# Kernel optimization log

Hardware: AMD Instinct MI355X
Metric: run time of the kernel (lower is better)

## Reference

```python
import jax, jax.numpy as jnp
import numpy as np

D_MODEL, N_HEADS, D_FF = 1024, 16, 4096
D_K = D_MODEL // N_HEADS
EPS = 1e-6


def _layernorm(x, alpha, bias):
    # Source uses mean and UNBIASED std (torch default), and adds eps to std (not var).
    mean = jnp.mean(x, axis=-1, keepdims=True)
    std = jnp.std(x, axis=-1, keepdims=True, ddof=1)
    return alpha * (x - mean) / (std + EPS) + bias


def setup_inputs() -> dict:
    key = jax.random.key(0)
    ks = jax.random.split(key, 16)
    B, S = 2, 2048
    s = 1.0 / np.sqrt(D_MODEL)
    inp = {
        "x": jax.random.normal(ks[0], (B, S, D_MODEL), dtype=jnp.float32),
        "mask": jnp.ones((1, 1, S, S), dtype=jnp.int32),
        # Linear weights stored as [d_in, d_out]
        "Wq": jax.random.normal(ks[1], (D_MODEL, D_MODEL), dtype=jnp.float32) * s,
        "bq": jnp.zeros((D_MODEL,), dtype=jnp.float32),
        "Wk": jax.random.normal(ks[2], (D_MODEL, D_MODEL), dtype=jnp.float32) * s,
        "bk": jnp.zeros((D_MODEL,), dtype=jnp.float32),
        "Wv": jax.random.normal(ks[3], (D_MODEL, D_MODEL), dtype=jnp.float32) * s,
        "bv": jnp.zeros((D_MODEL,), dtype=jnp.float32),
        "Wo": jax.random.normal(ks[4], (D_MODEL, D_MODEL), dtype=jnp.float32) * s,
        "bo": jnp.zeros((D_MODEL,), dtype=jnp.float32),
        "W1": jax.random.normal(ks[5], (D_MODEL, D_FF), dtype=jnp.float32) * s,
        "b1": jnp.zeros((D_FF,), dtype=jnp.float32),
        "W2": jax.random.normal(ks[6], (D_FF, D_MODEL), dtype=jnp.float32) / np.sqrt(D_FF),
        "b2": jnp.zeros((D_MODEL,), dtype=jnp.float32),
        "alpha1": jnp.ones((1,), dtype=jnp.float32),
        "beta1": jnp.zeros((1,), dtype=jnp.float32),
        "alpha2": jnp.ones((1,), dtype=jnp.float32),
        "beta2": jnp.zeros((1,), dtype=jnp.float32),
    }
    return inp


def reference(x, mask, Wq, bq, Wk, bk, Wv, bv, Wo, bo, W1, b1, W2, b2,
              alpha1, beta1, alpha2, beta2):
    # --- residual 1: pre-norm self-attention (dropout = identity in eval) ---
    xn = _layernorm(x, alpha1, beta1)
    B, S, _ = xn.shape
    q = (xn @ Wq + bq).reshape(B, S, N_HEADS, D_K).transpose(0, 2, 1, 3)  # [B,H,S,Dk]
    k = (xn @ Wk + bk).reshape(B, S, N_HEADS, D_K).transpose(0, 2, 1, 3)
    v = (xn @ Wv + bv).reshape(B, S, N_HEADS, D_K).transpose(0, 2, 1, 3)
    scores = jnp.einsum('bhqd,bhkd->bhqk', q, k) / np.sqrt(D_K)  # [B,H,S,S]
    scores = jnp.where(mask == 0, jnp.float32(-1e9), scores)
    attn = jax.nn.softmax(scores, axis=-1)
    ctx = jnp.einsum('bhqk,bhkd->bhqd', attn, v)
    ctx = ctx.transpose(0, 2, 1, 3).reshape(B, S, D_MODEL)
    attn_out = ctx @ Wo + bo
    x = x + attn_out

    # --- residual 2: pre-norm feed-forward ---
    xn = _layernorm(x, alpha2, beta2)
    ff = jax.nn.relu(xn @ W1 + b1) @ W2 + b2
    return x + ff
```

## Files before the change

kernel.cpp:

```cpp
#include <hip/hip_runtime.h>
#include <hip/hip_bf16.h>
#include <math.h>

#define SEQ   2048
#define BATCH 2
#define DMODEL 1024
#define NH    16
#define DKH   64
#define DFF   4096

typedef __attribute__((ext_vector_type(8))) short s16x8;
typedef __attribute__((ext_vector_type(4))) float f32x4;

__device__ __forceinline__ unsigned short f2bf(float f) {
  __hip_bfloat16 h = __float2bfloat16(f);
  return __builtin_bit_cast(unsigned short, h);
}

__device__ __forceinline__ unsigned cvt_pk_bf16(float lo, float hi) {
  unsigned r;
  asm("v_cvt_pk_bf16_f32 %0, %1, %2" : "=v"(r) : "v"(lo), "v"(hi));
  return r;
}

#define GLOAD16(g, l)                                                        \
  __builtin_amdgcn_global_load_lds(                                          \
      (const __attribute__((address_space(1))) void*)(g),                    \
      (__attribute__((address_space(3))) void*)(l), 16, 0, 0)

__global__ __launch_bounds__(256) void transpose_all_kernel(
    const float* __restrict__ Wq, const float* __restrict__ Wk,
    const float* __restrict__ Wv, const float* __restrict__ Wo,
    const float* __restrict__ W1, const float* __restrict__ W2,
    unsigned short* __restrict__ wq_t, unsigned short* __restrict__ wk_t,
    unsigned short* __restrict__ wv_t, unsigned short* __restrict__ wo_t,
    unsigned short* __restrict__ w1_t, unsigned short* __restrict__ w2_t) {
  const int id = blockIdx.x;
  const float* W; unsigned short* Wt; int K, N, t;
  if (id < 1024) {
    const int w = id >> 8; t = id & 255; K = DMODEL; N = DMODEL;
    W  = (w == 0) ? Wq : (w == 1) ? Wk : (w == 2) ? Wv : Wo;
    Wt = (w == 0) ? wq_t : (w == 1) ? wk_t : (w == 2) ? wv_t : wo_t;
  } else if (id < 2048) {
    t = id - 1024; K = DMODEL; N = DFF; W = W1; Wt = w1_t;
  } else {
    t = id - 2048; K = DFF; N = DMODEL; W = W2; Wt = w2_t;
  }
  const int nx = N / 64;
  const int n0 = (t % nx) * 64, k0 = (t / nx) * 64;
  __shared__ float tile[64][65];
  const int tx = threadIdx.x & 15, ty = threadIdx.x >> 4;
#pragma unroll
  for (int kk = 0; kk < 4; ++kk) {
    const int r = kk * 16 + ty;
    const float4 v = *reinterpret_cast<const float4*>(&W[(size_t)(k0 + r) * N + n0 + tx * 4]);
    tile[r][tx * 4 + 0] = v.x;
    tile[r][tx * 4 + 1] = v.y;
    tile[r][tx * 4 + 2] = v.z;
    tile[r][tx * 4 + 3] = v.w;
  }
  __syncthreads();
#pragma unroll
  for (int nn = 0; nn < 4; ++nn) {
    const int n = nn * 16 + ty;
    ushort4 o;
    o.x = f2bf(tile[tx * 4 + 0][n]);
    o.y = f2bf(tile[tx * 4 + 1][n]);
    o.z = f2bf(tile[tx * 4 + 2][n]);
    o.w = f2bf(tile[tx * 4 + 3][n]);
    *reinterpret_cast<ushort4*>(&Wt[(size_t)(n0 + n) * K + k0 + tx * 4]) = o;
  }
}

__global__ __launch_bounds__(256) void layernorm_kernel(
    const float* __restrict__ x, unsigned short* __restrict__ xn,
    const float* __restrict__ alpha, const float* __restrict__ beta) {
  const int row = blockIdx.x;
  const float4 v = reinterpret_cast<const float4*>(x + (size_t)row * DMODEL)[threadIdx.x];
  float s  = v.x + v.y + v.z + v.w;
  float ss = v.x * v.x + v.y * v.y + v.z * v.z + v.w * v.w;
#pragma unroll
  for (int off = 32; off; off >>= 1) {
    s  += __shfl_down(s, off);
    ss += __shfl_down(ss, off);
  }
  __shared__ float red[8];
  const int wv = threadIdx.x >> 6;
  if ((threadIdx.x & 63) == 0) { red[wv] = s; red[4 + wv] = ss; }
  __syncthreads();
  s  = red[0] + red[1] + red[2] + red[3];
  ss = red[4] + red[5] + red[6] + red[7];
  const float mean = s * (1.0f / DMODEL);
  float var = (ss - (float)DMODEL * mean * mean) * (1.0f / (DMODEL - 1));
  var = fmaxf(var, 0.0f);
  const float inv = alpha[0] / (sqrtf(var) + 1e-6f);
  const float b = beta[0] - mean * inv;
  ushort4 o;
  o.x = f2bf(v.x * inv + b);
  o.y = f2bf(v.y * inv + b);
  o.z = f2bf(v.z * inv + b);
  o.w = f2bf(v.w * inv + b);
  reinterpret_cast<ushort4*>(xn + (size_t)row * DMODEL)[threadIdx.x] = o;
}

template <bool RELU, bool RES, bool BIASM>
__global__ __launch_bounds__(256) void gemm_kernel(
    const unsigned short* __restrict__ A, const unsigned short* __restrict__ Bt,
    const float* __restrict__ bias, const float* __restrict__ res,
    void* __restrict__ out, int M, int N, int K, int ny) {
  __shared__ unsigned short a_lds[128][40];
  __shared__ unsigned short b_lds[128][40];
  const int bid = blockIdx.x;
  const int by = bid % ny, bx = bid / ny;
  const int m0 = by * 128, n0 = bx * 128;
  const int tid = threadIdx.x;
  const int lane = tid & 63, wave = tid >> 6;
  const int wm = wave >> 1, wn = wave & 1;
  const int l15 = lane & 15, lg = lane >> 4;
  const int srow = tid >> 2, scol = (tid & 3) * 8;

  f32x4 acc[4][4] = {};

  for (int k0 = 0; k0 < K; k0 += 32) {
    const int4 a0 = *reinterpret_cast<const int4*>(A + (size_t)(m0 + srow) * K + k0 + scol);
    const int4 a1 = *reinterpret_cast<const int4*>(A + (size_t)(m0 + srow + 64) * K + k0 + scol);
    const int4 b0 = *reinterpret_cast<const int4*>(Bt + (size_t)(n0 + srow) * K + k0 + scol);
    const int4 b1 = *reinterpret_cast<const int4*>(Bt + (size_t)(n0 + srow + 64) * K + k0 + scol);
    __syncthreads();
    *reinterpret_cast<int4*>(&a_lds[srow][scol])      = a0;
    *reinterpret_cast<int4*>(&a_lds[srow + 64][scol]) = a1;
    *reinterpret_cast<int4*>(&b_lds[srow][scol])      = b0;
    *reinterpret_cast<int4*>(&b_lds[srow + 64][scol]) = b1;
    __syncthreads();
    s16x8 af[4], bfr[4];
#pragma unroll
    for (int m = 0; m < 4; ++m)
      af[m] = *reinterpret_cast<const s16x8*>(&a_lds[wm * 64 + m * 16 + l15][lg * 8]);
#pragma unroll
    for (int n = 0; n < 4; ++n)
      bfr[n] = *reinterpret_cast<const s16x8*>(&b_lds[wn * 64 + n * 16 + l15][lg * 8]);
#pragma unroll
    for (int m = 0; m < 4; ++m)
#pragma unroll
      for (int n = 0; n < 4; ++n)
        acc[m][n] = __builtin_amdgcn_mfma_f32_16x16x32_bf16(af[m], bfr[n], acc[m][n], 0, 0, 0);
  }

#pragma unroll
  for (int m = 0; m < 4; ++m) {
#pragma unroll
    for (int n = 0; n < 4; ++n) {
      const int col = n0 + wn * 64 + n * 16 + l15;
      const float bcol = (bias && !BIASM) ? bias[col] : 0.0f;
#pragma unroll
      for (int r = 0; r < 4; ++r) {
        const int row = m0 + wm * 64 + m * 16 + 4 * lg + r;
        float v = acc[m][n][r] + (BIASM ? bias[row] : bcol);
        if (RELU) v = fmaxf(v, 0.0f);
        if (RES) {
          reinterpret_cast<float*>(out)[(size_t)row * N + col] =
              v + res[(size_t)row * N + col];
        } else {
          reinterpret_cast<unsigned short*>(out)[(size_t)row * N + col] = f2bf(v);
        }
      }
    }
  }
}

__global__ __launch_bounds__(512) void gemm8_kernel(
    const unsigned short* __restrict__ A, const unsigned short* __restrict__ Bt,
    const float* __restrict__ bias, const float* __restrict__ res,
    float* __restrict__ out, int M, int N, int K, int ny) {
  __shared__ unsigned short a_lds[2][128][40];
  __shared__ unsigned short b_lds[2][128][40];
  __shared__ float merge[32][132];
  const int bid = blockIdx.x;
  const int by = bid % ny, bx = bid / ny;
  const int m0 = by * 128, n0 = bx * 128;
  const int tid = threadIdx.x;
  const int g = tid >> 8;
  const int lt = tid & 255;
  const int lane = tid & 63, wave4 = (tid >> 6) & 3;
  const int wm = wave4 >> 1, wn = wave4 & 1;
  const int l15 = lane & 15, lg = lane >> 4;
  const int srow = lt >> 2, scol = (lt & 3) * 8;
  const int kbase = g * (K >> 1);

  f32x4 acc[4][4] = {};

  for (int k0 = 0; k0 < (K >> 1); k0 += 32) {
    const int ka = kbase + k0;
    const int4 a0 = *reinterpret_cast<const int4*>(A + (size_t)(m0 + srow) * K + ka + scol);
    const int4 a1 = *reinterpret_cast<const int4*>(A + (size_t)(m0 + srow + 64) * K + ka + scol);
    const int4 b0 = *reinterpret_cast<const int4*>(Bt + (size_t)(n0 + srow) * K + ka + scol);
    const int4 b1 = *reinterpret_cast<const int4*>(Bt + (size_t)(n0 + srow + 64) * K + ka + scol);
    __syncthreads();
    *reinterpret_cast<int4*>(&a_lds[g][srow][scol])      = a0;
    *reinterpret_cast<int4*>(&a_lds[g][srow + 64][scol]) = a1;
    *reinterpret_cast<int4*>(&b_lds[g][srow][scol])      = b0;
    *reinterpret_cast<int4*>(&b_lds[g][srow + 64][scol]) = b1;
    __syncthreads();
    s16x8 af[4], bfr[4];
#pragma unroll
    for (int m = 0; m < 4; ++m)
      af[m] = *reinterpret_cast<const s16x8*>(&a_lds[g][wm * 64 + m * 16 + l15][lg * 8]);
#pragma unroll
    for (int n = 0; n < 4; ++n)
      bfr[n] = *reinterpret_cast<const s16x8*>(&b_lds[g][wn * 64 + n * 16 + l15][lg * 8]);
#pragma unroll
    for (int m = 0; m < 4; ++m)
#pragma unroll
      for (int n = 0; n < 4; ++n)
        acc[m][n] = __builtin_amdgcn_mfma_f32_16x16x32_bf16(af[m], bfr[n], acc[m][n], 0, 0, 0);
  }

  __syncthreads();
#pragma unroll
  for (int c = 0; c < 4; ++c) {
    const int cwm = c >> 1;
    if (g == 1 && wm == cwm) {
#pragma unroll
      for (int mm = 0; mm < 2; ++mm) {
        const int m = 2 * (c & 1) + mm;
        const int lrow0 = m * 16 + 4 * lg - 32 * (c & 1);
#pragma unroll
        for (int n = 0; n < 4; ++n)
#pragma unroll
          for (int r = 0; r < 4; ++r)
            merge[lrow0 + r][wn * 64 + n * 16 + l15] = acc[m][n][r];
      }
    }
    __syncthreads();
    if (g == 0 && wm == cwm) {
#pragma unroll
      for (int mm = 0; mm < 2; ++mm) {
        const int m = 2 * (c & 1) + mm;
        const int lrow0 = m * 16 + 4 * lg - 32 * (c & 1);
#pragma unroll
        for (int n = 0; n < 4; ++n) {
          const int col = n0 + wn * 64 + n * 16 + l15;
          const float bcol = bias[col];
#pragma unroll
          for (int r = 0; r < 4; ++r) {
            const int row = m0 + wm * 64 + m * 16 + 4 * lg + r;
            out[(size_t)row * N + col] =
                acc[m][n][r] + merge[lrow0 + r][wn * 64 + n * 16 + l15] + bcol +
                res[(size_t)row * N + col];
          }
        }
      }
    }
    __syncthreads();
  }
}

__global__ __launch_bounds__(256) void qkv_kernel(
    const unsigned short* __restrict__ xn,
    const unsigned short* __restrict__ wq, const unsigned short* __restrict__ wk,
    const unsigned short* __restrict__ wv,
    const float* __restrict__ bq, const float* __restrict__ bk,
    const float* __restrict__ bv,
    unsigned short* __restrict__ Qb, unsigned short* __restrict__ Kb,
    unsigned short* __restrict__ Vtb) {
  __shared__ unsigned short a_lds[128][40];
  __shared__ unsigned short b_lds[128][40];
  const int bid = blockIdx.x;
  const int seg = bid >> 8, local = bid & 255;
  const unsigned short *A, *Bt; const float* bias; unsigned short* out;
  int N, by, bx; bool biasm;
  if (seg < 2) {
    A = xn; Bt = (seg == 0) ? wq : wk; bias = (seg == 0) ? bq : bk;
    out = (seg == 0) ? Qb : Kb;
    N = DMODEL; by = local % 32; bx = local / 32; biasm = false;
  } else {
    A = wv; Bt = xn; bias = bv; out = Vtb;
    N = BATCH * SEQ; by = local % 8; bx = local / 8; biasm = true;
  }
  const int K = DMODEL;
  const int m0 = by * 128, n0 = bx * 128;
  const int tid = threadIdx.x;
  const int lane = tid & 63, wave = tid >> 6;
  const int wm = wave >> 1, wn = wave & 1;
  const int l15 = lane & 15, lg = lane >> 4;
  const int srow = tid >> 2, scol = (tid & 3) * 8;

  f32x4 acc[4][4] = {};

  for (int k0 = 0; k0 < K; k0 += 32) {
    const int4 a0 = *reinterpret_cast<const int4*>(A + (size_t)(m0 + srow) * K + k0 + scol);
    const int4 a1 = *reinterpret_cast<const int4*>(A + (size_t)(m0 + srow + 64) * K + k0 + scol);
    const int4 b0 = *reinterpret_cast<const int4*>(Bt + (size_t)(n0 + srow) * K + k0 + scol);
    const int4 b1 = *reinterpret_cast<const int4*>(Bt + (size_t)(n0 + srow + 64) * K + k0 + scol);
    __syncthreads();
    *reinterpret_cast<int4*>(&a_lds[srow][scol])      = a0;
    *reinterpret_cast<int4*>(&a_lds[srow + 64][scol]) = a1;
    *reinterpret_cast<int4*>(&b_lds[srow][scol])      = b0;
    *reinterpret_cast<int4*>(&b_lds[srow + 64][scol]) = b1;
    __syncthreads();
    s16x8 af[4], bfr[4];
#pragma unroll
    for (int m = 0; m < 4; ++m)
      af[m] = *reinterpret_cast<const s16x8*>(&a_lds[wm * 64 + m * 16 + l15][lg * 8]);
#pragma unroll
    for (int n = 0; n < 4; ++n)
      bfr[n] = *reinterpret_cast<const s16x8*>(&b_lds[wn * 64 + n * 16 + l15][lg * 8]);
#pragma unroll
    for (int m = 0; m < 4; ++m)
#pragma unroll
      for (int n = 0; n < 4; ++n)
        acc[m][n] = __builtin_amdgcn_mfma_f32_16x16x32_bf16(af[m], bfr[n], acc[m][n], 0, 0, 0);
  }

#pragma unroll
  for (int m = 0; m < 4; ++m) {
#pragma unroll
    for (int n = 0; n < 4; ++n) {
      const int col = n0 + wn * 64 + n * 16 + l15;
      const float bcol = biasm ? 0.0f : bias[col];
#pragma unroll
      for (int r = 0; r < 4; ++r) {
        const int row = m0 + wm * 64 + m * 16 + 4 * lg + r;
        const float v = acc[m][n][r] + (biasm ? bias[row] : bcol);
        out[(size_t)row * N + col] = f2bf(v);
      }
    }
  }
}

__global__ __launch_bounds__(512) void attention_kernel(
    const unsigned short* __restrict__ Qg, const unsigned short* __restrict__ Kg,
    const unsigned short* __restrict__ Vt, unsigned short* __restrict__ Og) {
  __shared__ unsigned short K_lds[3][8][512];
  __shared__ unsigned short V_lds[3][8][512];
  __shared__ unsigned short Pt_lds[8][16][72];
  const int tid = threadIdx.x;
  const int lane = tid & 63, w = tid >> 6;
  const int l15 = lane & 15, lg = lane >> 4;
  const int bh = blockIdx.x, b = bh >> 4, h = bh & 15;
  const int q0 = blockIdx.y * 128;
  const size_t base = (size_t)b * SEQ * DMODEL + h * DKH;
  const unsigned short* vbase = Vt + (size_t)(h * DKH) * (BATCH * SEQ) + b * SEQ;

  const float SCALE = 0.125f * 1.44269504088896340736f;
  const int NT = SEQ / 64;

  const unsigned short* ksrc = Kg + base + (size_t)lane * DMODEL + w * 8;
  const unsigned short* vsrc = vbase + (size_t)lane * (BATCH * SEQ) + w * 8;

  s16x8 qf0, qf1;
  {
    const unsigned short* qp = Qg + base + (size_t)(q0 + w * 16 + l15) * DMODEL + lg * 8;
    qf0 = *reinterpret_cast<const s16x8*>(qp);
    qf1 = *reinterpret_cast<const s16x8*>(qp + 32);
#pragma unroll
    for (int i = 0; i < 8; ++i) {
      qf0[i] = (short)f2bf(__builtin_bit_cast(float, (unsigned)(unsigned short)qf0[i] << 16) * SCALE);
      qf1[i] = (short)f2bf(__builtin_bit_cast(float, (unsigned)(unsigned short)qf1[i] << 16) * SCALE);
    }
  }
  float lsum = 0.0f;
  f32x4 cacc[4] = {};

#define STAGE(buf, t)                                                         \
  do {                                                                        \
    GLOAD16(ksrc + (size_t)(t) * 64 * DMODEL, &K_lds[buf][w][0]);             \
    GLOAD16(vsrc + (t) * 64, &V_lds[buf][w][0]);                              \
  } while (0)

  STAGE(0, 0);
  STAGE(1, 1);
  asm volatile("s_waitcnt vmcnt(2)" ::: "memory");
  __builtin_amdgcn_s_barrier();
  __builtin_amdgcn_sched_barrier(0);

  int cb = 0;
  for (int t = 0; t < NT; ++t) {
    const bool pf = (t + 2 < NT);
    if (pf) {
      const int sb = (cb == 0) ? 2 : cb - 1;
      STAGE(sb, t + 2);
    }

#pragma unroll
    for (int nb = 0; nb < 4; ++nb) {
      const s16x8 kf0 = *reinterpret_cast<const s16x8*>(&K_lds[cb][lg][(nb * 16 + l15) * 8]);
      const s16x8 kf1 = *reinterpret_cast<const s16x8*>(&K_lds[cb][4 + lg][(nb * 16 + l15) * 8]);
      __builtin_amdgcn_s_setprio(1);
      f32x4 t4 = {};
      t4 = __builtin_amdgcn_mfma_f32_16x16x32_bf16(kf0, qf0, t4, 0, 0, 0);
      t4 = __builtin_amdgcn_mfma_f32_16x16x32_bf16(kf1, qf1, t4, 0, 0, 0);
      __builtin_amdgcn_s_setprio(0);
      const float p0 = exp2f(t4[0]), p1 = exp2f(t4[1]);
      const float p2 = exp2f(t4[2]), p3 = exp2f(t4[3]);
      lsum += (p0 + p1) + (p2 + p3);
      uint2 d;
      d.x = cvt_pk_bf16(p0, p1);
      d.y = cvt_pk_bf16(p2, p3);
      *reinterpret_cast<uint2*>(&Pt_lds[w][l15][nb * 16 + lg * 4]) = d;
    }

    const s16x8 pa0 = *reinterpret_cast<const s16x8*>(&Pt_lds[w][l15][lg * 8]);
    const s16x8 pa1 = *reinterpret_cast<const s16x8*>(&Pt_lds[w][l15][32 + lg * 8]);
    __builtin_amdgcn_s_setprio(1);
#pragma unroll
    for (int nb = 0; nb < 4; ++nb) {
      const s16x8 vf0 = *reinterpret_cast<const s16x8*>(&V_lds[cb][lg][(nb * 16 + l15) * 8]);
      const s16x8 vf1 = *reinterpret_cast<const s16x8*>(&V_lds[cb][4 + lg][(nb * 16 + l15) * 8]);
      cacc[nb] = __builtin_amdgcn_mfma_f32_16x16x32_bf16(pa0, vf0, cacc[nb], 0, 0, 0);
      cacc[nb] = __builtin_amdgcn_mfma_f32_16x16x32_bf16(pa1, vf1, cacc[nb], 0, 0, 0);
    }
    __builtin_amdgcn_s_setprio(0);

    if (t < NT - 1) {
      if (pf) {
        asm volatile("s_waitcnt vmcnt(2)" ::: "memory");
      } else {
        asm volatile("s_waitcnt vmcnt(0)" ::: "memory");
      }
      __builtin_amdgcn_s_barrier();
      __builtin_amdgcn_sched_barrier(0);
    }
    cb = (cb == 2) ? 0 : cb + 1;
  }
#undef STAGE

  lsum += __shfl_xor(lsum, 16);
  lsum += __shfl_xor(lsum, 32);
#pragma unroll
  for (int r = 0; r < 4; ++r) {
    const float dq = __shfl(lsum, lg * 4 + r);
    const float inv = 1.0f / dq;
    unsigned short* op = Og + base + (size_t)(q0 + w * 16 + lg * 4 + r) * DMODEL;
#pragma unroll
    for (int nb = 0; nb < 4; ++nb)
      op[nb * 16 + l15] = f2bf(cacc[nb][r] * inv);
  }
}

extern "C" void kernel_launch(void* const* d_in, const int* in_sizes, int n_in,
                              void* d_out, int out_size, void* d_ws, size_t ws_size,
                              hipStream_t stream) {
  const float* x  = (const float*)d_in[0];
  const float* Wq = (const float*)d_in[2];  const float* bq = (const float*)d_in[3];
  const float* Wk = (const float*)d_in[4];  const float* bk = (const float*)d_in[5];
  const float* Wv = (const float*)d_in[6];  const float* bv = (const float*)d_in[7];
  const float* Wo = (const float*)d_in[8];  const float* bo = (const float*)d_in[9];
  const float* W1 = (const float*)d_in[10]; const float* b1 = (const float*)d_in[11];
  const float* W2 = (const float*)d_in[12]; const float* b2 = (const float*)d_in[13];
  const float* alpha1 = (const float*)d_in[14]; const float* beta1 = (const float*)d_in[15];
  const float* alpha2 = (const float*)d_in[16]; const float* beta2 = (const float*)d_in[17];

  char* ws = (char*)d_ws;
  unsigned short* wq_t = (unsigned short*)(ws + (size_t)(0ull  << 20));
  unsigned short* wk_t = (unsigned short*)(ws + (size_t)(2ull  << 20));
  unsigned short* wv_t = (unsigned short*)(ws + (size_t)(4ull  << 20));
  unsigned short* wo_t = (unsigned short*)(ws + (size_t)(6ull  << 20));
  unsigned short* w1_t = (unsigned short*)(ws + (size_t)(8ull  << 20));
  unsigned short* w2_t = (unsigned short*)(ws + (size_t)(16ull << 20));
  unsigned short* xn   = (unsigned short*)(ws + (size_t)(24ull << 20));
  unsigned short* Qb   = (unsigned short*)(ws + (size_t)(32ull << 20));
  unsigned short* Kb   = (unsigned short*)(ws + (size_t)(40ull << 20));
  unsigned short* Vtb  = (unsigned short*)(ws + (size_t)(48ull << 20));
  unsigned short* ctxb = (unsigned short*)(ws + (size_t)(56ull << 20));
  float*          x1   = (float*)(ws + (size_t)(64ull << 20));
  unsigned short* hb   = (unsigned short*)(ws + (size_t)(32ull << 20));

  const dim3 blk(256);
  const int M = BATCH * SEQ;

  transpose_all_kernel<<<3072, blk, 0, stream>>>(Wq, Wk, Wv, Wo, W1, W2,
                                                 wq_t, wk_t, wv_t, wo_t, w1_t, w2_t);

  layernorm_kernel<<<M, blk, 0, stream>>>(x, xn, alpha1, beta1);

  qkv_kernel<<<768, blk, 0, stream>>>(xn, wq_t, wk_t, wv_t, bq, bk, bv, Qb, Kb, Vtb);

  attention_kernel<<<dim3(BATCH * NH, SEQ / 128), dim3(512), 0, stream>>>(Qb, Kb, Vtb, ctxb);

  gemm8_kernel<<<256, dim3(512), 0, stream>>>(ctxb, wo_t, bo, x, x1, M, DMODEL, DMODEL, 32);

  layernorm_kernel<<<M, blk, 0, stream>>>(x1, xn, alpha2, beta2);

  gemm_kernel<true, false, false><<<1024, blk, 0, stream>>>(xn, w1_t, b1, nullptr, hb, M, DFF, DMODEL, 32);

  gemm8_kernel<<<256, dim3(512), 0, stream>>>(hb, w2_t, b2, x1, (float*)d_out, M, DMODEL, DFF, 32);
}
```

Before: 277.5 us.

## Split-K the FFN down-projection into four partial GEMMs plus a reduce kernel

Replaces the 256-block gemm8 down-projection (K=4096) with a split-K scheme: 1024 blocks each compute a 128x128 tile over a quarter of K, write bf16 partials to workspace, and a separate reduce kernel sums them with bias and residual. The aim is to fill more compute units than 256 blocks can. In exchange it adds partial-buffer traffic, an extra launch, a simple non-double-buffered main loop, and bf16 rounding of the partials before summation. It only runs when the workspace is large enough.

New measurement: 273.7 us. No clear change (-1.4%).

```diff
diff --git a/kernel.cpp b/kernel.cpp
--- a/kernel.cpp
+++ b/kernel.cpp
@@ -15,6 +15,10 @@
 __device__ __forceinline__ unsigned short f2bf(float f) {
   __hip_bfloat16 h = __float2bfloat16(f);
   return __builtin_bit_cast(unsigned short, h);
+}
+
+__device__ __forceinline__ float bf2f(unsigned short u) {
+  return __builtin_bit_cast(float, (unsigned)u << 16);
 }
 
 __device__ __forceinline__ unsigned cvt_pk_bf16(float lo, float hi) {
@@ -166,6 +170,86 @@
       }
     }
   }
+}
+
+__global__ __launch_bounds__(256) void gemm_part_kernel(
+    const unsigned short* __restrict__ A, const unsigned short* __restrict__ Bt,
+    unsigned short* __restrict__ part) {
+  __shared__ unsigned short a_lds[128][40];
+  __shared__ unsigned short b_lds[128][40];
+  const int bid = blockIdx.x;
+  const int ks = bid >> 8, local = bid & 255;
+  const int by = local % 32, bx = local / 32;
+  const int m0 = by * 128, n0 = bx * 128;
+  const int koff = ks * 1024;
+  const int tid = threadIdx.x;
+  const int lane = tid & 63, wave = tid >> 6;
+  const int wm = wave >> 1, wn = wave & 1;
+  const int l15 = lane & 15, lg = lane >> 4;
+  const int srow = tid >> 2, scol = (tid & 3) * 8;
+  unsigned short* pout = part + (size_t)ks * ((size_t)(BATCH * SEQ) * DMODEL);
+
+  f32x4 acc[4][4] = {};
+
+  for (int k0 = 0; k0 < 1024; k0 += 32) {
+    const int4 a0 = *reinterpret_cast<const int4*>(A + (size_t)(m0 + srow) * DFF + koff + k0 + scol);
+    const int4 a1 = *reinterpret_cast<const int4*>(A + (size_t)(m0 + srow + 64) * DFF + koff + k0 + scol);
+    const int4 b0 = *reinterpret_cast<const int4*>(Bt + (size_t)(n0 + srow) * DFF + koff + k0 + scol);
+    const int4 b1 = *reinterpret_cast<const int4*>(Bt + (size_t)(n0 + srow + 64) * DFF + koff + k0 + scol);
+    __syncthreads();
+    *reinterpret_cast<int4*>(&a_lds[srow][scol])      = a0;
+    *reinterpret_cast<int4*>(&a_lds[srow + 64][scol]) = a1;
+    *reinterpret_cast<int4*>(&b_lds[srow][scol])      = b0;
+    *reinterpret_cast<int4*>(&b_lds[srow + 64][scol]) = b1;
+    __syncthreads();
+    s16x8 af[4], bfr[4];
+#pragma unroll
+    for (int m = 0; m < 4; ++m)
+      af[m] = *reinterpret_cast<const s16x8*>(&a_lds[wm * 64 + m * 16 + l15][lg * 8]);
+#pragma unroll
+    for (int n = 0; n < 4; ++n)
+      bfr[n] = *reinterpret_cast<const s16x8*>(&b_lds[wn * 64 + n * 16 + l15][lg * 8]);
+#pragma unroll
+    for (int m = 0; m < 4; ++m)
+#pragma unroll
+      for (int n = 0; n < 4; ++n)
+        acc[m][n] = __builtin_amdgcn_mfma_f32_16x16x32_bf16(af[m], bfr[n], acc[m][n], 0, 0, 0);
+  }
+
+#pragma unroll
+  for (int m = 0; m < 4; ++m)
+#pragma unroll
+    for (int n = 0; n < 4; ++n) {
+      const int col = n0 + wn * 64 + n * 16 + l15;
+#pragma unroll
+      for (int r = 0; r < 4; ++r) {
+        const int row = m0 + wm * 64 + m * 16 + 4 * lg + r;
+        pout[(size_t)row * DMODEL + col] = f2bf(acc[m][n][r]);
+      }
+    }
+}
+
+__global__ __launch_bounds__(256) void reduce4_kernel(
+    const unsigned short* __restrict__ part, const float* __restrict__ bias,
+    const float* __restrict__ res, float* __restrict__ out) {
+  const size_t TOT = (size_t)(BATCH * SEQ) * DMODEL;
+  const size_t j = (size_t)blockIdx.x * 256 + threadIdx.x;
+  const size_t off = j * 4;
+  if (off >= TOT) return;
+  float4 s = {0.f, 0.f, 0.f, 0.f};
+#pragma unroll
+  for (int ks = 0; ks < 4; ++ks) {
+    const ushort4 v = *reinterpret_cast<const ushort4*>(part + ks * TOT + off);
+    s.x += bf2f(v.x); s.y += bf2f(v.y); s.z += bf2f(v.z); s.w += bf2f(v.w);
+  }
+  const float4 bi = *reinterpret_cast<const float4*>(bias + (off & (DMODEL - 1)));
+  const float4 rr = *reinterpret_cast<const float4*>(res + off);
+  float4 o;
+  o.x = s.x + bi.x + rr.x;
+  o.y = s.y + bi.y + rr.y;
+  o.z = s.z + bi.z + rr.z;
+  o.w = s.w + bi.w + rr.w;
+  *reinterpret_cast<float4*>(out + off) = o;
 }
 
 __global__ __launch_bounds__(512) void gemm8_kernel(
@@ -465,9 +549,11 @@
   unsigned short* ctxb = (unsigned short*)(ws + (size_t)(56ull << 20));
   float*          x1   = (float*)(ws + (size_t)(64ull << 20));
   unsigned short* hb   = (unsigned short*)(ws + (size_t)(32ull << 20));
+  unsigned short* pbuf = (unsigned short*)(ws + (size_t)(80ull << 20));
 
   const dim3 blk(256);
   const int M = BATCH * SEQ;
+  const bool big_ws = ws_size >= (112ull << 20);
 
   transpose_all_kernel<<<3072, blk, 0, stream>>>(Wq, Wk, Wv, Wo, W1, W2,
                                                  wq_t, wk_t, wv_t, wo_t, w1_t, w2_t);
@@ -484,5 +570,10 @@
 
   gemm_kernel<true, false, false><<<1024, blk, 0, stream>>>(xn, w1_t, b1, nullptr, hb, M, DFF, DMODEL, 32);
 
-  gemm8_kernel<<<256, dim3(512), 0, stream>>>(hb, w2_t, b2, x1, (float*)d_out, M, DMODEL, DFF, 32);
-}
+  if (big_ws) {
+    gemm_part_kernel<<<1024, blk, 0, stream>>>(hb, w2_t, pbuf);
+    reduce4_kernel<<<4096, blk, 0, stream>>>(pbuf, b2, x1, (float*)d_out);
+  } else {
+    gemm8_kernel<<<256, dim3(512), 0, stream>>>(hb, w2_t, b2, x1, (float*)d_out, M, DMODEL, DFF, 32);
+  }
+}
```
